# Kernel optimization log

Hardware: AMD Instinct MI355X
Metric: run time of the kernel (lower is better)

The kernel has to match this reference:

```python
import jax, jax.numpy as jnp
import numpy as np

N_NODES = 50000
N_EDGES = 800000
IN_FEAT = 64
HIDDEN = 128
NUM_LAYERS = 3


def setup_inputs() -> dict:
    key = jax.random.key(0)
    ks = jax.random.split(key, 8)
    x = jax.random.normal(ks[0], (N_NODES, IN_FEAT), dtype=jnp.float32)
    edge_index = jax.random.randint(ks[1], (2, N_EDGES), 0, N_NODES, dtype=jnp.int64)
    s_in = 1.0 / np.sqrt(IN_FEAT)
    s_h = 1.0 / np.sqrt(HIDDEN)
    W_in = jax.random.uniform(ks[2], (IN_FEAT, HIDDEN), jnp.float32, -s_in, s_in)
    b_in = jax.random.uniform(ks[3], (HIDDEN,), jnp.float32, -s_in, s_in)
    W_self = jax.random.uniform(ks[4], (NUM_LAYERS, HIDDEN, HIDDEN), jnp.float32, -s_h, s_h)
    b_self = jax.random.uniform(ks[5], (NUM_LAYERS, HIDDEN), jnp.float32, -s_h, s_h)
    W_nbr = jax.random.uniform(ks[6], (NUM_LAYERS, HIDDEN, HIDDEN), jnp.float32, -s_h, s_h)
    return {"x": x, "edge_index": edge_index, "W_in": W_in, "b_in": b_in,
            "W_self": W_self, "b_self": b_self, "W_nbr": W_nbr}


def reference(x, edge_index, W_in, b_in, W_self, b_self, W_nbr):
    # input projection: h [N, HIDDEN]
    h = x @ W_in + b_in
    src = edge_index[0]
    dst = edge_index[1]
    n = h.shape[0]
    ones = jnp.ones((dst.shape[0], 1), dtype=h.dtype)
    # scatter-mean denominator is grad-constant; compute once
    cnt = jax.ops.segment_sum(ones, dst, num_segments=n)
    cnt = jnp.maximum(cnt, 1.0)
    for l in range(W_self.shape[0]):
        msg = h[src] @ W_nbr[l]                               # [E, HIDDEN]
        agg = jax.ops.segment_sum(msg, dst, num_segments=n) / cnt  # scatter-mean
        h = jax.nn.elu(h @ W_self[l] + b_self[l] + agg)
    return h
```

## Files before the change

### kernel.cpp

```cpp
#include <hip/hip_runtime.h>
#include <cstdint>

#define HIDDEN 128
#define NC 128
#define NR 8
#define MAXNPR 6400

typedef unsigned short u16;
using frag_t   = __attribute__((ext_vector_type(8))) short;
using f32x4_t  = __attribute__((ext_vector_type(4))) float;
using ushort8_t = __attribute__((ext_vector_type(8))) unsigned short;

__device__ __forceinline__ float bf2f(u16 u) {
    union { unsigned int i; float f; } c;
    c.i = ((unsigned int)u) << 16;
    return c.f;
}
__device__ __forceinline__ u16 f2bf(float f) {
    unsigned int u = __float_as_uint(f);
    unsigned int r = (u + 0x7fffu + ((u >> 16) & 1u)) >> 16;
    return (u16)r;
}


__global__ __launch_bounds__(256) void k_hist2_prep(
    const int* __restrict__ ei, int E, u16* __restrict__ counts, int npr, int n,
    const float* __restrict__ x,
    const float* __restrict__ W_in,
    const float* __restrict__ W_self,
    const float* __restrict__ W_nbr,
    u16* __restrict__ xf,
    u16* __restrict__ WtI_hi, u16* __restrict__ WtI_lo,
    u16* __restrict__ WtS_hi, u16* __restrict__ WtS_lo,
    u16* __restrict__ WtN_hi, u16* __restrict__ WtN_lo,
    int L, int nxg)
{
    __shared__ int lh[MAXNPR];
    int r = blockIdx.x & (NR - 1);
    int j = blockIdx.x >> 3;
    int lo = r * npr;
    int hi = lo + npr; if (hi > n) hi = n;
    int nr = hi - lo;
    for (int i = threadIdx.x; i < nr; i += 256) lh[i] = 0;
    __syncthreads();

    int nch4 = E >> 2;
    int c0 = (int)((long long)j * nch4 / NC);
    int c1 = (int)((long long)(j + 1) * nch4 / NC);
    const int4* d4 = (const int4*)(ei + E);
    for (int c = c0 + threadIdx.x; c < c1; c += 256) {
        int4 d = d4[c];
        if (d.x >= lo && d.x < hi) atomicAdd(&lh[d.x - lo], 1);
        if (d.y >= lo && d.y < hi) atomicAdd(&lh[d.y - lo], 1);
        if (d.z >= lo && d.z < hi) atomicAdd(&lh[d.z - lo], 1);
        if (d.w >= lo && d.w < hi) atomicAdd(&lh[d.w - lo], 1);
    }
    if (j == NC - 1 && (E & 3)) {
        for (int e = (nch4 << 2) + threadIdx.x; e < E; e += 256) {
            int d = ei[E + e];
            if (d >= lo && d < hi) atomicAdd(&lh[d - lo], 1);
        }
    }
    __syncthreads();
    for (int i = threadIdx.x; i < nr; i += 256)
        counts[(size_t)j * n + lo + i] = (u16)lh[i];

    {
        int nIn = 64 * 128;
        int nSq = L * 128 * 128;
        int wtot = nIn + 2 * nSq;
        int total = wtot + nxg;
        int stride = gridDim.x * blockDim.x;
        for (int i = blockIdx.x * blockDim.x + threadIdx.x; i < total; i += stride) {
            if (i >= wtot) {
                int t = i - wtot;
                int row = t >> 3, c = t & 7;
                const float4* xs = (const float4*)(x + (size_t)row * 64 + c * 8);
                float4 v0 = xs[0], v1 = xs[1];
                ushort8_t o;
                o[0] = f2bf(v0.x); o[1] = f2bf(v0.y); o[2] = f2bf(v0.z); o[3] = f2bf(v0.w);
                o[4] = f2bf(v1.x); o[5] = f2bf(v1.y); o[6] = f2bf(v1.z); o[7] = f2bf(v1.w);
                int T = row >> 4, m = row & 15;
                int f = c >> 2, q = c & 3;
                *(ushort8_t*)&xf[((size_t)(T * 2 + f) * 64 + q * 16 + m) * 8] = o;
            } else {
                float v; u16* phi; u16* plo; int o;
                if (i < nIn) {
                    int nn = i / 64, k = i % 64;
                    v = W_in[k * 128 + nn]; phi = WtI_hi; plo = WtI_lo; o = nn * 64 + k;
                } else if (i < nIn + nSq) {
                    int t = i - nIn;
                    int l = t / (128 * 128), rr = t % (128 * 128);
                    int nn = rr / 128, k = rr % 128;
                    v = W_self[l * 128 * 128 + k * 128 + nn]; phi = WtS_hi; plo = WtS_lo;
                    o = l * 128 * 128 + nn * 128 + k;
                } else {
                    int t = i - nIn - nSq;
                    int l = t / (128 * 128), rr = t % (128 * 128);
                    int nn = rr / 128, k = rr % 128;
                    v = W_nbr[l * 128 * 128 + k * 128 + nn]; phi = WtN_hi; plo = WtN_lo;
                    o = l * 128 * 128 + nn * 128 + k;
                }
                u16 hiv = f2bf(v);
                phi[o] = hiv;
                plo[o] = f2bf(v - bf2f(hiv));
            }
        }
    }
}


__global__ void k_deg_scan(const u16* __restrict__ counts, u16* __restrict__ base,
                           int* __restrict__ rowp, int* __restrict__ bsums, int n) {
    __shared__ int sh[1024];
    int t = threadIdx.x;
    int v = blockIdx.x * 1024 + t;
    int run = 0;
    if (v < n) {
#pragma unroll 8
        for (int j = 0; j < NC; ++j) {
            int c = counts[(size_t)j * n + v];
            base[(size_t)j * n + v] = (u16)run;
            run += c;
        }
    }
    sh[t] = run;
    __syncthreads();
    for (int off = 1; off < 1024; off <<= 1) {
        int xx = sh[t];
        int y = (t >= off) ? sh[t - off] : 0;
        __syncthreads();
        sh[t] = xx + y;
        __syncthreads();
    }
    if (v < n) rowp[v + 1] = sh[t];
    if (t == 1023) bsums[blockIdx.x] = sh[1023];
}

__global__ void k_scan_tail(int* __restrict__ rowp, const int* __restrict__ bsums,
                            int n, int nb) {
    __shared__ int sh[1024];
    int t = threadIdx.x;
    int b = blockIdx.x;
    sh[t] = (t < nb) ? bsums[t] : 0;
    __syncthreads();
    for (int off = 1; off < 1024; off <<= 1) {
        int xx = sh[t];
        int y = (t >= off) ? sh[t - off] : 0;
        __syncthreads();
        sh[t] = xx + y;
        __syncthreads();
    }
    int boff = (b == 0) ? 0 : sh[b - 1];
    int bb = b * 1024;
    if (bb + t < n) rowp[bb + t + 1] += boff;
    if (b == 0 && t == 0) rowp[0] = 0;
}


__device__ __forceinline__ void dev_fill2(const int* __restrict__ ei, int E,
                                          const int* __restrict__ rowp,
                                          const u16* __restrict__ base,
                                          int* __restrict__ colx,
                                          int npr, int n, int bid, int* lh) {
    int r = bid & (NR - 1);
    int j = bid >> 3;
    int lo = r * npr;
    int hi = lo + npr; if (hi > n) hi = n;
    int nr = hi - lo;
    for (int i = threadIdx.x; i < nr; i += 256) lh[i] = 0;
    __syncthreads();

    int nch4 = E >> 2;
    int c0 = (int)((long long)j * nch4 / NC);
    int c1 = (int)((long long)(j + 1) * nch4 / NC);
    const int4* s4 = (const int4*)ei;
    const int4* d4 = (const int4*)(ei + E);
    const u16* basej = base + (size_t)j * n;
    for (int c = c0 + threadIdx.x; c < c1; c += 256) {
        int4 d = d4[c];
        bool m0 = d.x >= lo && d.x < hi;
        bool m1 = d.y >= lo && d.y < hi;
        bool m2 = d.z >= lo && d.z < hi;
        bool m3 = d.w >= lo && d.w < hi;
        if (m0 | m1 | m2 | m3) {
            int4 s = s4[c];
            if (m0) { int sl = atomicAdd(&lh[d.x - lo], 1); colx[rowp[d.x] + (int)basej[d.x] + sl] = s.x; }
            if (m1) { int sl = atomicAdd(&lh[d.y - lo], 1); colx[rowp[d.y] + (int)basej[d.y] + sl] = s.y; }
            if (m2) { int sl = atomicAdd(&lh[d.z - lo], 1); colx[rowp[d.z] + (int)basej[d.z] + sl] = s.z; }
            if (m3) { int sl = atomicAdd(&lh[d.w - lo], 1); colx[rowp[d.w] + (int)basej[d.w] + sl] = s.w; }
        }
    }
    if (j == NC - 1 && (E & 3)) {
        for (int e = (nch4 << 2) + threadIdx.x; e < E; e += 256) {
            int d = ei[E + e];
            if (d >= lo && d < hi) {
                int sl = atomicAdd(&lh[d - lo], 1);
                colx[rowp[d] + (int)basej[d] + sl] = ei[e];
            }
        }
    }
}


__global__ __launch_bounds__(256, 4) void k_agg(
        const ushort8_t* __restrict__ hb8, const int* __restrict__ rowp,
        const int* __restrict__ colx, u16* __restrict__ Sf, int n) {
    int g = (blockIdx.x * blockDim.x + threadIdx.x) >> 4;
    int lane = threadIdx.x & 15;
    if (g >= n) return;
    int beg = rowp[g];
    int end = rowp[g + 1];
    float a0[8], a1[8];
#pragma unroll
    for (int j = 0; j < 8; ++j) { a0[j] = 0.f; a1[j] = 0.f; }
    int e = beg;
    for (; e + 15 < end; e += 16) {
        int s0 = colx[e],      s1 = colx[e + 1],  s2 = colx[e + 2],  s3 = colx[e + 3];
        int s4 = colx[e + 4],  s5 = colx[e + 5],  s6 = colx[e + 6],  s7 = colx[e + 7];
        int s8 = colx[e + 8],  s9 = colx[e + 9],  sa = colx[e + 10], sb = colx[e + 11];
        int sc = colx[e + 12], sd = colx[e + 13], se = colx[e + 14], sf = colx[e + 15];
        ushort8_t v0 = hb8[(size_t)s0 * 16 + lane];
        ushort8_t v1 = hb8[(size_t)s1 * 16 + lane];
        ushort8_t v2 = hb8[(size_t)s2 * 16 + lane];
        ushort8_t v3 = hb8[(size_t)s3 * 16 + lane];
        ushort8_t v4 = hb8[(size_t)s4 * 16 + lane];
        ushort8_t v5 = hb8[(size_t)s5 * 16 + lane];
        ushort8_t v6 = hb8[(size_t)s6 * 16 + lane];
        ushort8_t v7 = hb8[(size_t)s7 * 16 + lane];
        ushort8_t v8 = hb8[(size_t)s8 * 16 + lane];
        ushort8_t v9 = hb8[(size_t)s9 * 16 + lane];
        ushort8_t va = hb8[(size_t)sa * 16 + lane];
        ushort8_t vb = hb8[(size_t)sb * 16 + lane];
        ushort8_t vc = hb8[(size_t)sc * 16 + lane];
        ushort8_t vd = hb8[(size_t)sd * 16 + lane];
        ushort8_t ve = hb8[(size_t)se * 16 + lane];
        ushort8_t vf = hb8[(size_t)sf * 16 + lane];
#pragma unroll
        for (int j = 0; j < 8; ++j) {
            a0[j] += bf2f(v0[j]); a1[j] += bf2f(v1[j]);
            a0[j] += bf2f(v2[j]); a1[j] += bf2f(v3[j]);
            a0[j] += bf2f(v4[j]); a1[j] += bf2f(v5[j]);
            a0[j] += bf2f(v6[j]); a1[j] += bf2f(v7[j]);
        }
#pragma unroll
        for (int j = 0; j < 8; ++j) {
            a0[j] += bf2f(v8[j]); a1[j] += bf2f(v9[j]);
            a0[j] += bf2f(va[j]); a1[j] += bf2f(vb[j]);
            a0[j] += bf2f(vc[j]); a1[j] += bf2f(vd[j]);
            a0[j] += bf2f(ve[j]); a1[j] += bf2f(vf[j]);
        }
    }
    for (; e + 7 < end; e += 8) {
        int s0 = colx[e],     s1 = colx[e + 1], s2 = colx[e + 2], s3 = colx[e + 3];
        int s4 = colx[e + 4], s5 = colx[e + 5], s6 = colx[e + 6], s7 = colx[e + 7];
        ushort8_t v0 = hb8[(size_t)s0 * 16 + lane];
        ushort8_t v1 = hb8[(size_t)s1 * 16 + lane];
        ushort8_t v2 = hb8[(size_t)s2 * 16 + lane];
        ushort8_t v3 = hb8[(size_t)s3 * 16 + lane];
        ushort8_t v4 = hb8[(size_t)s4 * 16 + lane];
        ushort8_t v5 = hb8[(size_t)s5 * 16 + lane];
        ushort8_t v6 = hb8[(size_t)s6 * 16 + lane];
        ushort8_t v7 = hb8[(size_t)s7 * 16 + lane];
#pragma unroll
        for (int j = 0; j < 8; ++j) {
            a0[j] += bf2f(v0[j]); a1[j] += bf2f(v1[j]);
            a0[j] += bf2f(v2[j]); a1[j] += bf2f(v3[j]);
            a0[j] += bf2f(v4[j]); a1[j] += bf2f(v5[j]);
            a0[j] += bf2f(v6[j]); a1[j] += bf2f(v7[j]);
        }
    }
    for (; e + 3 < end; e += 4) {
        int s0 = colx[e], s1 = colx[e + 1], s2 = colx[e + 2], s3 = colx[e + 3];
        ushort8_t v0 = hb8[(size_t)s0 * 16 + lane];
        ushort8_t v1 = hb8[(size_t)s1 * 16 + lane];
        ushort8_t v2 = hb8[(size_t)s2 * 16 + lane];
        ushort8_t v3 = hb8[(size_t)s3 * 16 + lane];
#pragma unroll
        for (int j = 0; j < 8; ++j) {
            a0[j] += bf2f(v0[j]); a1[j] += bf2f(v1[j]);
            a0[j] += bf2f(v2[j]); a1[j] += bf2f(v3[j]);
        }
    }
    for (; e < end; ++e) {
        int s = colx[e];
        ushort8_t v = hb8[(size_t)s * 16 + lane];
#pragma unroll
        for (int j = 0; j < 8; ++j) a0[j] += bf2f(v[j]);
    }
    int deg = end - beg;
    float inv = 1.0f / (float)(deg > 1 ? deg : 1);
    ushort8_t o;
#pragma unroll
    for (int j = 0; j < 8; ++j) o[j] = f2bf((a0[j] + a1[j]) * inv);
    int T = g >> 4, m = g & 15;
    *(ushort8_t*)&Sf[((size_t)(T * 4 + (lane >> 2)) * 64 + (lane & 3) * 16 + m) * 8] = o;
}


template <int KF1, int KF2, int DO_ELU>
__device__ __forceinline__ void dev_gemm(
    const u16* __restrict__ A1f, const u16* __restrict__ A2f,
    const u16* __restrict__ B1h, const u16* __restrict__ B1l,
    const u16* __restrict__ B2h, const u16* __restrict__ B2l,
    const float* __restrict__ bias, float* __restrict__ C,
    u16* __restrict__ Hrow, u16* __restrict__ Hf,
    int M, int bid, int gdim)
{
    constexpr int K1 = KF1 * 32;
    constexpr int K2 = KF2 * 32;
    constexpr int KF = KF1 + KF2;
    int lane = threadIdx.x & 63;
    int w    = threadIdx.x >> 6;
    int m16  = lane & 15;
    int quad = lane >> 4;
    int kq   = quad * 8;
    int ng   = (bid >> 3) & 1;
    int mtb  = (bid & 7) | ((bid >> 4) << 3);
    int ncol = (ng * 4 + w) * 16 + m16;

    frag_t bh[KF], bl[KF];
    if constexpr (KF1 > 0) {
#pragma unroll
        for (int f = 0; f < KF1; ++f) {
            bh[f] = *(const frag_t*)&B1h[(size_t)ncol * K1 + f * 32 + kq];
            bl[f] = *(const frag_t*)&B1l[(size_t)ncol * K1 + f * 32 + kq];
        }
    }
    if constexpr (KF2 > 0) {
#pragma unroll
        for (int f = 0; f < KF2; ++f) {
            bh[KF1 + f] = *(const frag_t*)&B2h[(size_t)ncol * K2 + f * 32 + kq];
            bl[KF1 + f] = *(const frag_t*)&B2l[(size_t)ncol * K2 + f * 32 + kq];
        }
    }

    float bv = bias[ncol];
    int nMT  = (M + 31) >> 5;
    int step = gdim >> 1;
    int fcol = ncol >> 5;
    int qcol = (ncol & 31) >> 3;
    int jcol = ncol & 7;

    auto loadA = [&](int mt, frag_t (&a0)[KF], frag_t (&a1)[KF]) {
        int T0 = mt * 2, T1 = T0 + 1;
        if constexpr (KF1 > 0) {
#pragma unroll
            for (int f = 0; f < KF1; ++f) {
                a0[f] = *(const frag_t*)&A1f[((size_t)(T0 * KF1 + f) * 64 + lane) * 8];
                a1[f] = *(const frag_t*)&A1f[((size_t)(T1 * KF1 + f) * 64 + lane) * 8];
            }
        }
        if constexpr (KF2 > 0) {
#pragma unroll
            for (int f = 0; f < KF2; ++f) {
                a0[KF1 + f] = *(const frag_t*)&A2f[((size_t)(T0 * KF2 + f) * 64 + lane) * 8];
                a1[KF1 + f] = *(const frag_t*)&A2f[((size_t)(T1 * KF2 + f) * 64 + lane) * 8];
            }
        }
    };

    auto compute = [&](int mt, frag_t (&a0)[KF], frag_t (&a1)[KF]) {
        f32x4_t acc0 = (f32x4_t){0.f, 0.f, 0.f, 0.f};
        f32x4_t acc1 = (f32x4_t){0.f, 0.f, 0.f, 0.f};
#pragma unroll
        for (int f = 0; f < KF; ++f) {
            acc0 = __builtin_amdgcn_mfma_f32_16x16x32_bf16(a0[f], bh[f], acc0, 0, 0, 0);
            acc1 = __builtin_amdgcn_mfma_f32_16x16x32_bf16(a1[f], bh[f], acc1, 0, 0, 0);
            acc0 = __builtin_amdgcn_mfma_f32_16x16x32_bf16(a0[f], bl[f], acc0, 0, 0, 0);
            acc1 = __builtin_amdgcn_mfma_f32_16x16x32_bf16(a1[f], bl[f], acc1, 0, 0, 0);
        }
        int rb = mt * 32 + quad * 4;
#pragma unroll
        for (int r = 0; r < 4; ++r) {
#pragma unroll
            for (int half = 0; half < 2; ++half) {
                int row = rb + r + half * 16;
                float av = half ? acc1[r] : acc0[r];
                if (row < M) {
                    float v = av + bv;
                    if constexpr (DO_ELU) v = (v > 0.f) ? v : expm1f(v);
                    if (C) C[(size_t)row * HIDDEN + ncol] = v;
                    if (Hrow) {
                        u16 hv = f2bf(v);
                        Hrow[(size_t)row * HIDDEN + ncol] = hv;
                        Hf[((size_t)((row >> 4) * 4 + fcol) * 64 + qcol * 16 + (row & 15)) * 8 + jcol] = hv;
                    }
                }
            }
        }
    };

    int mt = mtb;
    if (mt < nMT) {
        frag_t xa0[KF], xa1[KF], ya0[KF], ya1[KF];
        loadA(mt, xa0, xa1);
        while (true) {
            int mt2 = mt + step;
            if (mt2 < nMT) loadA(mt2, ya0, ya1);
            compute(mt, xa0, xa1);
            if (mt2 >= nMT) break;
            int mt3 = mt2 + step;
            if (mt3 < nMT) loadA(mt3, xa0, xa1);
            compute(mt2, ya0, ya1);
            if (mt3 >= nMT) break;
            mt = mt3;
        }
    }
}

template <int KF1, int KF2, int DO_ELU>
__global__ __launch_bounds__(256, 2) void k_gemm_mfma(
    const u16* __restrict__ A1f, const u16* __restrict__ A2f,
    const u16* __restrict__ B1h, const u16* __restrict__ B1l,
    const u16* __restrict__ B2h, const u16* __restrict__ B2l,
    const float* __restrict__ bias, float* __restrict__ C,
    u16* __restrict__ Hrow, u16* __restrict__ Hf, int M)
{
    dev_gemm<KF1, KF2, DO_ELU>(A1f, A2f, B1h, B1l, B2h, B2l, bias, C, Hrow, Hf,
                               M, blockIdx.x, gridDim.x);
}


__global__ __launch_bounds__(256, 2) void k_fill2_gemm(
    const int* __restrict__ ei, int E,
    const int* __restrict__ rowp, const u16* __restrict__ base,
    int* __restrict__ colx, int npr, int n, int nbF,
    const u16* __restrict__ xf,
    const u16* __restrict__ WtI_hi, const u16* __restrict__ WtI_lo,
    const float* __restrict__ b_in,
    u16* __restrict__ hRow, u16* __restrict__ hf, int M, int gdim)
{
    __shared__ int cur[MAXNPR];
    if (blockIdx.x < (unsigned)nbF) {
        dev_fill2(ei, E, rowp, base, colx, npr, n, blockIdx.x, cur);
    } else {
        dev_gemm<2, 0, 0>(xf, nullptr, WtI_hi, WtI_lo, nullptr, nullptr,
                          b_in, nullptr, hRow, hf, M, blockIdx.x - nbF, gdim);
    }
}


extern "C" void kernel_launch(void* const* d_in, const int* in_sizes, int n_in,
                              void* d_out, int out_size, void* d_ws, size_t ws_size,
                              hipStream_t stream) {
    const float* x        = (const float*)d_in[0];
    const int* ei         = (const int*)d_in[1];
    const float* W_in     = (const float*)d_in[2];
    const float* b_in     = (const float*)d_in[3];
    const float* W_self   = (const float*)d_in[4];
    const float* b_self   = (const float*)d_in[5];
    const float* W_nbr    = (const float*)d_in[6];
    float* out = (float*)d_out;

    const int IN_FEAT = 64;
    int N = in_sizes[0] / IN_FEAT;
    int E = in_sizes[1] / 2;
    int L = in_sizes[4] / (HIDDEN * HIDDEN);

    char* ws = (char*)d_ws;
    size_t off = 0;
    auto alloc = [&](size_t bytes) -> void* {
        void* p = ws + off;
        off = (off + bytes + 255) & ~(size_t)255;
        return p;
    };

    int nT = ((N + 31) / 32) * 2;

    u16* hRowA = (u16*)alloc((size_t)N * HIDDEN * 2);
    u16* hRowB = (u16*)alloc((size_t)N * HIDDEN * 2);
    u16* hfA   = (u16*)alloc((size_t)nT * 4 * 64 * 8 * 2);
    u16* hfB   = (u16*)alloc((size_t)nT * 4 * 64 * 8 * 2);
    u16* xf    = (u16*)alloc((size_t)nT * 2 * 64 * 8 * 2);
    u16* Sf    = (u16*)alloc((size_t)nT * 4 * 64 * 8 * 2);
    u16* WtI_hi = (u16*)alloc(128 * 64 * 2);
    u16* WtI_lo = (u16*)alloc(128 * 64 * 2);
    u16* WtS_hi = (u16*)alloc((size_t)L * 128 * 128 * 2);
    u16* WtS_lo = (u16*)alloc((size_t)L * 128 * 128 * 2);
    u16* WtN_hi = (u16*)alloc((size_t)L * 128 * 128 * 2);
    u16* WtN_lo = (u16*)alloc((size_t)L * 128 * 128 * 2);
    u16* counts = (u16*)alloc((size_t)NC * N * sizeof(u16));
    u16* base   = (u16*)alloc((size_t)NC * N * sizeof(u16));
    int* rowp  = (int*)alloc((size_t)(N + 1) * sizeof(int));
    int* colx  = (int*)alloc((size_t)E * sizeof(int));
    int* bsums = (int*)alloc(1024 * sizeof(int));

    int npr = (N + NR - 1) / NR;

    k_hist2_prep<<<NR * NC, 256, 0, stream>>>(ei, E, counts, npr, N,
                                              x, W_in, W_self, W_nbr, xf,
                                              WtI_hi, WtI_lo, WtS_hi, WtS_lo,
                                              WtN_hi, WtN_lo, L, N * 8);
    int nb = (N + 1023) / 1024;
    k_deg_scan<<<nb, 1024, 0, stream>>>(counts, base, rowp, bsums, N);
    k_scan_tail<<<nb, 1024, 0, stream>>>(rowp, bsums, N, nb);

    const int GB = 1024;
    const int NBF = NR * NC;

    k_fill2_gemm<<<NBF + GB, 256, 0, stream>>>(
        ei, E, rowp, base, colx, npr, N, NBF,
        xf, WtI_hi, WtI_lo, b_in, hRowA, hfA, N, GB);

    u16* curRow = hRowA; u16* curF = hfA;
    u16* nxtRow = hRowB; u16* nxtF = hfB;

    for (int l = 0; l < L; ++l) {
        k_agg<<<(N + 15) / 16, 256, 0, stream>>>((const ushort8_t*)curRow, rowp, colx, Sf, N);
        const u16* Wsh = WtS_hi + (size_t)l * 128 * 128;
        const u16* Wsl = WtS_lo + (size_t)l * 128 * 128;
        const u16* Wnh = WtN_hi + (size_t)l * 128 * 128;
        const u16* Wnl = WtN_lo + (size_t)l * 128 * 128;
        const float* bs = b_self + (size_t)l * HIDDEN;
        bool last = (l == L - 1);
        k_gemm_mfma<4, 4, 1><<<GB, 256, 0, stream>>>(
            curF, Sf,
            Wsh, Wsl, Wnh, Wnl,
            bs, last ? out : nullptr,
            last ? nullptr : nxtRow, last ? nullptr : nxtF, N);
        u16* tr = curRow; curRow = nxtRow; nxtRow = tr;
        u16* tf = curF;   curF = nxtF;     nxtF = tf;
    }
}
```

Measured before the change: 290.3 us.

## Fuse neighbor aggregation and layer GEMM into one per-tile kernel

Replaces the separate gather-mean kernel and MFMA GEMM kernel with a single kernel per 32-node tile. The block computes the self GEMM, gathers neighbor features into shared memory in fragment layout, syncs, and then runs the neighbor GEMM before the ELU epilogue. This removes the global Sf round trip and one launch per layer. In exchange, weights are reloaded from global memory by every one of roughly 1563 blocks, and the persistent double-buffered A-prefetch loop is gone.

```diff
diff --git a/kernel.cpp b/kernel.cpp
--- a/kernel.cpp
+++ b/kernel.cpp
@@ -203,101 +203,6 @@
 }
 
 
-__global__ __launch_bounds__(256, 4) void k_agg(
-        const ushort8_t* __restrict__ hb8, const int* __restrict__ rowp,
-        const int* __restrict__ colx, u16* __restrict__ Sf, int n) {
-    int g = (blockIdx.x * blockDim.x + threadIdx.x) >> 4;
-    int lane = threadIdx.x & 15;
-    if (g >= n) return;
-    int beg = rowp[g];
-    int end = rowp[g + 1];
-    float a0[8], a1[8];
-#pragma unroll
-    for (int j = 0; j < 8; ++j) { a0[j] = 0.f; a1[j] = 0.f; }
-    int e = beg;
-    for (; e + 15 < end; e += 16) {
-        int s0 = colx[e],      s1 = colx[e + 1],  s2 = colx[e + 2],  s3 = colx[e + 3];
-        int s4 = colx[e + 4],  s5 = colx[e + 5],  s6 = colx[e + 6],  s7 = colx[e + 7];
-        int s8 = colx[e + 8],  s9 = colx[e + 9],  sa = colx[e + 10], sb = colx[e + 11];
-        int sc = colx[e + 12], sd = colx[e + 13], se = colx[e + 14], sf = colx[e + 15];
-        ushort8_t v0 = hb8[(size_t)s0 * 16 + lane];
-        ushort8_t v1 = hb8[(size_t)s1 * 16 + lane];
-        ushort8_t v2 = hb8[(size_t)s2 * 16 + lane];
-        ushort8_t v3 = hb8[(size_t)s3 * 16 + lane];
-        ushort8_t v4 = hb8[(size_t)s4 * 16 + lane];
-        ushort8_t v5 = hb8[(size_t)s5 * 16 + lane];
-        ushort8_t v6 = hb8[(size_t)s6 * 16 + lane];
-        ushort8_t v7 = hb8[(size_t)s7 * 16 + lane];
-        ushort8_t v8 = hb8[(size_t)s8 * 16 + lane];
-        ushort8_t v9 = hb8[(size_t)s9 * 16 + lane];
-        ushort8_t va = hb8[(size_t)sa * 16 + lane];
-        ushort8_t vb = hb8[(size_t)sb * 16 + lane];
-        ushort8_t vc = hb8[(size_t)sc * 16 + lane];
-        ushort8_t vd = hb8[(size_t)sd * 16 + lane];
-        ushort8_t ve = hb8[(size_t)se * 16 + lane];
-        ushort8_t vf = hb8[(size_t)sf * 16 + lane];
-#pragma unroll
-        for (int j = 0; j < 8; ++j) {
-            a0[j] += bf2f(v0[j]); a1[j] += bf2f(v1[j]);
-            a0[j] += bf2f(v2[j]); a1[j] += bf2f(v3[j]);
-            a0[j] += bf2f(v4[j]); a1[j] += bf2f(v5[j]);
-            a0[j] += bf2f(v6[j]); a1[j] += bf2f(v7[j]);
-        }
-#pragma unroll
-        for (int j = 0; j < 8; ++j) {
-            a0[j] += bf2f(v8[j]); a1[j] += bf2f(v9[j]);
-            a0[j] += bf2f(va[j]); a1[j] += bf2f(vb[j]);
-            a0[j] += bf2f(vc[j]); a1[j] += bf2f(vd[j]);
-            a0[j] += bf2f(ve[j]); a1[j] += bf2f(vf[j]);
-        }
-    }
-    for (; e + 7 < end; e += 8) {
-        int s0 = colx[e],     s1 = colx[e + 1], s2 = colx[e + 2], s3 = colx[e + 3];
-        int s4 = colx[e + 4], s5 = colx[e + 5], s6 = colx[e + 6], s7 = colx[e + 7];
-        ushort8_t v0 = hb8[(size_t)s0 * 16 + lane];
-        ushort8_t v1 = hb8[(size_t)s1 * 16 + lane];
-        ushort8_t v2 = hb8[(size_t)s2 * 16 + lane];
-        ushort8_t v3 = hb8[(size_t)s3 * 16 + lane];
-        ushort8_t v4 = hb8[(size_t)s4 * 16 + lane];
-        ushort8_t v5 = hb8[(size_t)s5 * 16 + lane];
-        ushort8_t v6 = hb8[(size_t)s6 * 16 + lane];
-        ushort8_t v7 = hb8[(size_t)s7 * 16 + lane];
-#pragma unroll
-        for (int j = 0; j < 8; ++j) {
-            a0[j] += bf2f(v0[j]); a1[j] += bf2f(v1[j]);
-            a0[j] += bf2f(v2[j]); a1[j] += bf2f(v3[j]);
-            a0[j] += bf2f(v4[j]); a1[j] += bf2f(v5[j]);
-            a0[j] += bf2f(v6[j]); a1[j] += bf2f(v7[j]);
-        }
-    }
-    for (; e + 3 < end; e += 4) {
-        int s0 = colx[e], s1 = colx[e + 1], s2 = colx[e + 2], s3 = colx[e + 3];
-        ushort8_t v0 = hb8[(size_t)s0 * 16 + lane];
-        ushort8_t v1 = hb8[(size_t)s1 * 16 + lane];
-        ushort8_t v2 = hb8[(size_t)s2 * 16 + lane];
-        ushort8_t v3 = hb8[(size_t)s3 * 16 + lane];
-#pragma unroll
-        for (int j = 0; j < 8; ++j) {
-            a0[j] += bf2f(v0[j]); a1[j] += bf2f(v1[j]);
-            a0[j] += bf2f(v2[j]); a1[j] += bf2f(v3[j]);
-        }
-    }
-    for (; e < end; ++e) {
-        int s = colx[e];
-        ushort8_t v = hb8[(size_t)s * 16 + lane];
-#pragma unroll
-        for (int j = 0; j < 8; ++j) a0[j] += bf2f(v[j]);
-    }
-    int deg = end - beg;
-    float inv = 1.0f / (float)(deg > 1 ? deg : 1);
-    ushort8_t o;
-#pragma unroll
-    for (int j = 0; j < 8; ++j) o[j] = f2bf((a0[j] + a1[j]) * inv);
-    int T = g >> 4, m = g & 15;
-    *(ushort8_t*)&Sf[((size_t)(T * 4 + (lane >> 2)) * 64 + (lane & 3) * 16 + m) * 8] = o;
-}
-
-
 template <int KF1, int KF2, int DO_ELU>
 __device__ __forceinline__ void dev_gemm(
     const u16* __restrict__ A1f, const u16* __restrict__ A2f,
@@ -409,18 +314,6 @@
     }
 }
 
-template <int KF1, int KF2, int DO_ELU>
-__global__ __launch_bounds__(256, 2) void k_gemm_mfma(
-    const u16* __restrict__ A1f, const u16* __restrict__ A2f,
-    const u16* __restrict__ B1h, const u16* __restrict__ B1l,
-    const u16* __restrict__ B2h, const u16* __restrict__ B2l,
-    const float* __restrict__ bias, float* __restrict__ C,
-    u16* __restrict__ Hrow, u16* __restrict__ Hf, int M)
-{
-    dev_gemm<KF1, KF2, DO_ELU>(A1f, A2f, B1h, B1l, B2h, B2l, bias, C, Hrow, Hf,
-                               M, blockIdx.x, gridDim.x);
-}
-
 
 __global__ __launch_bounds__(256, 2) void k_fill2_gemm(
     const int* __restrict__ ei, int E,
@@ -441,6 +334,191 @@
 }
 
 
+__global__ __launch_bounds__(512, 2) void k_layer2(
+    const ushort8_t* __restrict__ hb8,
+    const u16* __restrict__ Af,
+    const int* __restrict__ rowp, const int* __restrict__ colx,
+    const u16* __restrict__ Bsh, const u16* __restrict__ Bsl,
+    const u16* __restrict__ Bnh, const u16* __restrict__ Bnl,
+    const float* __restrict__ bias,
+    float* __restrict__ C, u16* __restrict__ Hrow, u16* __restrict__ Hf,
+    int M)
+{
+    __shared__ u16 sf[2 * 4 * 64 * 8];
+    int mt   = blockIdx.x;
+    int tid  = threadIdx.x;
+    int lane = tid & 63;
+    int w    = tid >> 6;
+    int m16  = lane & 15;
+    int quad = lane >> 4;
+    int kq   = quad * 8;
+    int ncol = w * 16 + m16;
+
+    f32x4_t acc0 = (f32x4_t){0.f, 0.f, 0.f, 0.f};
+    f32x4_t acc1 = (f32x4_t){0.f, 0.f, 0.f, 0.f};
+
+    {
+        frag_t bh[4], bl[4], a0[4], a1[4];
+        int T0 = mt * 2, T1 = T0 + 1;
+#pragma unroll
+        for (int f = 0; f < 4; ++f) {
+            bh[f] = *(const frag_t*)&Bsh[(size_t)ncol * 128 + f * 32 + kq];
+            bl[f] = *(const frag_t*)&Bsl[(size_t)ncol * 128 + f * 32 + kq];
+            a0[f] = *(const frag_t*)&Af[((size_t)(T0 * 4 + f) * 64 + lane) * 8];
+            a1[f] = *(const frag_t*)&Af[((size_t)(T1 * 4 + f) * 64 + lane) * 8];
+        }
+#pragma unroll
+        for (int f = 0; f < 4; ++f) {
+            acc0 = __builtin_amdgcn_mfma_f32_16x16x32_bf16(a0[f], bh[f], acc0, 0, 0, 0);
+            acc1 = __builtin_amdgcn_mfma_f32_16x16x32_bf16(a1[f], bh[f], acc1, 0, 0, 0);
+            acc0 = __builtin_amdgcn_mfma_f32_16x16x32_bf16(a0[f], bl[f], acc0, 0, 0, 0);
+            acc1 = __builtin_amdgcn_mfma_f32_16x16x32_bf16(a1[f], bl[f], acc1, 0, 0, 0);
+        }
+    }
+
+    {
+        int anode = tid >> 4;
+        int alane = tid & 15;
+        int g = mt * 32 + anode;
+        ushort8_t o;
+        if (g < M) {
+            int beg = rowp[g];
+            int end = rowp[g + 1];
+            float ag0[8], ag1[8];
+#pragma unroll
+            for (int j = 0; j < 8; ++j) { ag0[j] = 0.f; ag1[j] = 0.f; }
+            int e = beg;
+            for (; e + 15 < end; e += 16) {
+                int s0 = colx[e],      s1 = colx[e + 1],  s2 = colx[e + 2],  s3 = colx[e + 3];
+                int s4 = colx[e + 4],  s5 = colx[e + 5],  s6 = colx[e + 6],  s7 = colx[e + 7];
+                int s8 = colx[e + 8],  s9 = colx[e + 9],  sa = colx[e + 10], sb = colx[e + 11];
+                int sc = colx[e + 12], sd = colx[e + 13], se = colx[e + 14], sf_ = colx[e + 15];
+                ushort8_t v0 = hb8[(size_t)s0 * 16 + alane];
+                ushort8_t v1 = hb8[(size_t)s1 * 16 + alane];
+                ushort8_t v2 = hb8[(size_t)s2 * 16 + alane];
+                ushort8_t v3 = hb8[(size_t)s3 * 16 + alane];
+                ushort8_t v4 = hb8[(size_t)s4 * 16 + alane];
+                ushort8_t v5 = hb8[(size_t)s5 * 16 + alane];
+                ushort8_t v6 = hb8[(size_t)s6 * 16 + alane];
+                ushort8_t v7 = hb8[(size_t)s7 * 16 + alane];
+                ushort8_t v8 = hb8[(size_t)s8 * 16 + alane];
+                ushort8_t v9 = hb8[(size_t)s9 * 16 + alane];
+                ushort8_t va = hb8[(size_t)sa * 16 + alane];
+                ushort8_t vb = hb8[(size_t)sb * 16 + alane];
+                ushort8_t vc = hb8[(size_t)sc * 16 + alane];
+                ushort8_t vd = hb8[(size_t)sd * 16 + alane];
+                ushort8_t ve = hb8[(size_t)se * 16 + alane];
+                ushort8_t vf = hb8[(size_t)sf_ * 16 + alane];
+#pragma unroll
+                for (int j = 0; j < 8; ++j) {
+                    ag0[j] += bf2f(v0[j]); ag1[j] += bf2f(v1[j]);
+                    ag0[j] += bf2f(v2[j]); ag1[j] += bf2f(v3[j]);
+                    ag0[j] += bf2f(v4[j]); ag1[j] += bf2f(v5[j]);
+                    ag0[j] += bf2f(v6[j]); ag1[j] += bf2f(v7[j]);
+                }
+#pragma unroll
+                for (int j = 0; j < 8; ++j) {
+                    ag0[j] += bf2f(v8[j]); ag1[j] += bf2f(v9[j]);
+                    ag0[j] += bf2f(va[j]); ag1[j] += bf2f(vb[j]);
+                    ag0[j] += bf2f(vc[j]); ag1[j] += bf2f(vd[j]);
+                    ag0[j] += bf2f(ve[j]); ag1[j] += bf2f(vf[j]);
+                }
+            }
+            for (; e + 7 < end; e += 8) {
+                int s0 = colx[e],     s1 = colx[e + 1], s2 = colx[e + 2], s3 = colx[e + 3];
+                int s4 = colx[e + 4], s5 = colx[e + 5], s6 = colx[e + 6], s7 = colx[e + 7];
+                ushort8_t v0 = hb8[(size_t)s0 * 16 + alane];
+                ushort8_t v1 = hb8[(size_t)s1 * 16 + alane];
+                ushort8_t v2 = hb8[(size_t)s2 * 16 + alane];
+                ushort8_t v3 = hb8[(size_t)s3 * 16 + alane];
+                ushort8_t v4 = hb8[(size_t)s4 * 16 + alane];
+                ushort8_t v5 = hb8[(size_t)s5 * 16 + alane];
+                ushort8_t v6 = hb8[(size_t)s6 * 16 + alane];
+                ushort8_t v7 = hb8[(size_t)s7 * 16 + alane];
+#pragma unroll
+                for (int j = 0; j < 8; ++j) {
+                    ag0[j] += bf2f(v0[j]); ag1[j] += bf2f(v1[j]);
+                    ag0[j] += bf2f(v2[j]); ag1[j] += bf2f(v3[j]);
+                    ag0[j] += bf2f(v4[j]); ag1[j] += bf2f(v5[j]);
+                    ag0[j] += bf2f(v6[j]); ag1[j] += bf2f(v7[j]);
+                }
+            }
+            for (; e + 3 < end; e += 4) {
+                int s0 = colx[e], s1 = colx[e + 1], s2 = colx[e + 2], s3 = colx[e + 3];
+                ushort8_t v0 = hb8[(size_t)s0 * 16 + alane];
+                ushort8_t v1 = hb8[(size_t)s1 * 16 + alane];
+                ushort8_t v2 = hb8[(size_t)s2 * 16 + alane];
+                ushort8_t v3 = hb8[(size_t)s3 * 16 + alane];
+#pragma unroll
+                for (int j = 0; j < 8; ++j) {
+                    ag0[j] += bf2f(v0[j]); ag1[j] += bf2f(v1[j]);
+                    ag0[j] += bf2f(v2[j]); ag1[j] += bf2f(v3[j]);
+                }
+            }
+            for (; e < end; ++e) {
+                int s = colx[e];
+                ushort8_t v = hb8[(size_t)s * 16 + alane];
+#pragma unroll
+                for (int j = 0; j < 8; ++j) ag0[j] += bf2f(v[j]);
+            }
+            int deg = end - beg;
+            float inv = 1.0f / (float)(deg > 1 ? deg : 1);
+#pragma unroll
+            for (int j = 0; j < 8; ++j) o[j] = f2bf((ag0[j] + ag1[j]) * inv);
+        } else {
+#pragma unroll
+            for (int j = 0; j < 8; ++j) o[j] = 0;
+        }
+        *(ushort8_t*)&sf[(((anode >> 4) * 4 + (alane >> 2)) * 64 + (alane & 3) * 16 + (anode & 15)) * 8] = o;
+    }
+    __syncthreads();
+
+    {
+        frag_t bh[4], bl[4], a0[4], a1[4];
+#pragma unroll
+        for (int f = 0; f < 4; ++f) {
+            bh[f] = *(const frag_t*)&Bnh[(size_t)ncol * 128 + f * 32 + kq];
+            bl[f] = *(const frag_t*)&Bnl[(size_t)ncol * 128 + f * 32 + kq];
+            a0[f] = *(const frag_t*)&sf[((0 * 4 + f) * 64 + lane) * 8];
+            a1[f] = *(const frag_t*)&sf[((1 * 4 + f) * 64 + lane) * 8];
+        }
+#pragma unroll
+        for (int f = 0; f < 4; ++f) {
+            acc0 = __builtin_amdgcn_mfma_f32_16x16x32_bf16(a0[f], bh[f], acc0, 0, 0, 0);
+            acc1 = __builtin_amdgcn_mfma_f32_16x16x32_bf16(a1[f], bh[f], acc1, 0, 0, 0);
+            acc0 = __builtin_amdgcn_mfma_f32_16x16x32_bf16(a0[f], bl[f], acc0, 0, 0, 0);
+            acc1 = __builtin_amdgcn_mfma_f32_16x16x32_bf16(a1[f], bl[f], acc1, 0, 0, 0);
+        }
+    }
+
+    {
+        float bv = bias[ncol];
+        int fcol = ncol >> 5;
+        int qcol = (ncol & 31) >> 3;
+        int jcol = ncol & 7;
+        int rb = mt * 32 + quad * 4;
+#pragma unroll
+        for (int r = 0; r < 4; ++r) {
+#pragma unroll
+            for (int half = 0; half < 2; ++half) {
+                int row = rb + r + half * 16;
+                float av = half ? acc1[r] : acc0[r];
+                if (row < M) {
+                    float v = av + bv;
+                    v = (v > 0.f) ? v : expm1f(v);
+                    if (C) C[(size_t)row * HIDDEN + ncol] = v;
+                    if (Hrow) {
+                        u16 hv = f2bf(v);
+                        Hrow[(size_t)row * HIDDEN + ncol] = hv;
+                        Hf[((size_t)((row >> 4) * 4 + fcol) * 64 + qcol * 16 + (row & 15)) * 8 + jcol] = hv;
+                    }
+                }
+            }
+        }
+    }
+}
+
+
 extern "C" void kernel_launch(void* const* d_in, const int* in_sizes, int n_in,
                               void* d_out, int out_size, void* d_ws, size_t ws_size,
                               hipStream_t stream) {
@@ -473,7 +551,6 @@
     u16* hfA   = (u16*)alloc((size_t)nT * 4 * 64 * 8 * 2);
     u16* hfB   = (u16*)alloc((size_t)nT * 4 * 64 * 8 * 2);
     u16* xf    = (u16*)alloc((size_t)nT * 2 * 64 * 8 * 2);
-    u16* Sf    = (u16*)alloc((size_t)nT * 4 * 64 * 8 * 2);
     u16* WtI_hi = (u16*)alloc(128 * 64 * 2);
     u16* WtI_lo = (u16*)alloc(128 * 64 * 2);
     u16* WtS_hi = (u16*)alloc((size_t)L * 128 * 128 * 2);
@@ -506,18 +583,18 @@
     u16* curRow = hRowA; u16* curF = hfA;
     u16* nxtRow = hRowB; u16* nxtF = hfB;
 
+    int nTiles = (N + 31) / 32;
     for (int l = 0; l < L; ++l) {
-        k_agg<<<(N + 15) / 16, 256, 0, stream>>>((const ushort8_t*)curRow, rowp, colx, Sf, N);
         const u16* Wsh = WtS_hi + (size_t)l * 128 * 128;
         const u16* Wsl = WtS_lo + (size_t)l * 128 * 128;
         const u16* Wnh = WtN_hi + (size_t)l * 128 * 128;
         const u16* Wnl = WtN_lo + (size_t)l * 128 * 128;
         const float* bs = b_self + (size_t)l * HIDDEN;
         bool last = (l == L - 1);
-        k_gemm_mfma<4, 4, 1><<<GB, 256, 0, stream>>>(
-            curF, Sf,
-            Wsh, Wsl, Wnh, Wnl,
-            bs, last ? out : nullptr,
+        k_layer2<<<nTiles, 512, 0, stream>>>(
+            (const ushort8_t*)curRow, curF, rowp, colx,
+            Wsh, Wsl, Wnh, Wnl, bs,
+            last ? out : nullptr,
             last ? nullptr : nxtRow, last ? nullptr : nxtF, N);
         u16* tr = curRow; curRow = nxtRow; nxtRow = tr;
         u16* tf = curF;   curF = nxtF;     nxtF = tf;
```

After: 331.8 us. 1.14x slower.
